# Optimization experiments

Hardware: AMD Instinct MI355X
Metric: run time of the kernel (lower is better)

## Reference

```python
import jax, jax.numpy as jnp
import numpy as np

B = 8192        # batch
DB = 64         # dim_body
DO = 128        # dim_object
NOBJ = 9        # nb_objects (all connected)
NE = 72         # edges = NOBJ*(NOBJ-1)
DE = 128        # edge feature dim
NISO = 3        # isolated nodes
HID = 256
PHI_OUT = 256
ACT = 32
LOG_SIG_MIN, LOG_SIG_MAX = -20.0, 2.0


def setup_inputs() -> dict:
    key = jax.random.key(0)
    ks = jax.random.split(key, 16)
    s = 0.05
    return {
        "obs": jax.random.normal(ks[0], (B, DB + NOBJ * DO), jnp.float32),
        "edge_features": jax.random.normal(ks[1], (B, NE, DE), jnp.float32),
        # every object id 0..8 appears NE//NOBJ times (static edge targets)
        "edges_to": jnp.tile(jnp.arange(NOBJ, dtype=jnp.int32), NE // NOBJ),
        "isolated_nodes": jax.random.normal(ks[2], (B, NISO, DO), jnp.float32),
        "isolated_nodes_features": jax.random.normal(ks[3], (B, NISO, DE), jnp.float32),
        "W1_phi": jax.random.normal(ks[4], (DB + DO + DE, HID), jnp.float32) * s,
        "b1_phi": jnp.zeros((HID,), jnp.float32),
        "W2_phi": jax.random.normal(ks[5], (HID, PHI_OUT), jnp.float32) * s,
        "b2_phi": jnp.zeros((PHI_OUT,), jnp.float32),
        "W1_rho": jax.random.normal(ks[6], (PHI_OUT, HID), jnp.float32) * s,
        "b1_rho": jnp.zeros((HID,), jnp.float32),
        "Wm": jax.random.normal(ks[7], (HID, ACT), jnp.float32) * s,
        "bm": jnp.zeros((ACT,), jnp.float32),
        "Ws": jax.random.normal(ks[8], (HID, ACT), jnp.float32) * s,
        "bs": jnp.zeros((ACT,), jnp.float32),
    }


def reference(obs, edge_features, edges_to, isolated_nodes, isolated_nodes_features,
              W1_phi, b1_phi, W2_phi, b2_phi, W1_rho, b1_rho, Wm, bm, Ws, bs):
    obs_body = obs[:, :DB]                              # [B, DB]
    obs_objects = obs[:, DB:].reshape(B, NOBJ, DO)      # [B, NOBJ, DO]

    # per-node max over incoming edges (segment-max over static edge targets)
    ef = jnp.transpose(edge_features, (1, 0, 2))        # [NE, B, DE]
    incoming = jax.ops.segment_max(ef, edges_to, num_segments=NOBJ)  # [NOBJ, B, DE]

    body_c = jnp.broadcast_to(obs_body, (NOBJ, B, DB))
    inp_connected = jnp.concatenate(
        [body_c, jnp.transpose(obs_objects, (1, 0, 2)), incoming], axis=-1)

    body_i = jnp.broadcast_to(obs_body, (NISO, B, DB))
    inp_isolated = jnp.concatenate(
        [body_i,
         jnp.transpose(isolated_nodes, (1, 0, 2)),
         jnp.transpose(isolated_nodes_features, (1, 0, 2))], axis=-1)

    inp = jnp.concatenate([inp_connected, inp_isolated], axis=0)  # [NOBJ+NISO, B, DB+DO+DE]

    # phi DeepSet MLP
    h = jax.nn.relu(inp @ W1_phi + b1_phi)
    phi = jax.nn.relu(h @ W2_phi + b2_phi)

    pooled = phi.sum(axis=0)                            # readout='sum' -> [B, PHI_OUT]

    # rho MLP -> (mean, log_std)
    r = jax.nn.relu(pooled @ W1_rho + b1_rho)
    mean = r @ Wm + bm
    log_std = jnp.clip(r @ Ws + bs, LOG_SIG_MIN, LOG_SIG_MAX)
    return mean, log_std
```

## Files before the change

### kernel.cpp

```cpp
#include <hip/hip_runtime.h>
#include <hip/hip_bf16.h>
#include <stdint.h>


#define Bsz   8192
#define OBSW  1216
#define NH    256

typedef unsigned short u16;
typedef unsigned int   u32;

using bf16x8 = __attribute__((ext_vector_type(8))) short;
using f32x4  = __attribute__((ext_vector_type(4))) float;

__device__ u16   g_W1t[256 * 320];
__device__ u16   g_W2t[256 * 256];
__device__ u16   g_Rt [256 * 256];
__device__ u16   g_Wcat[64 * 256];
__device__ float g_pooled[Bsz * NH];

__device__ __forceinline__ u16 f2bf(float f) {
  union { float f; u32 i; } v; v.f = f;
  u32 x = v.i;
  x += 0x7fffu + ((x >> 16) & 1u);
  return (u16)(x >> 16);
}
__device__ __forceinline__ uint4 pack8(const float* f) {
  uint4 o;
  o.x = (u32)f2bf(f[0]) | ((u32)f2bf(f[1]) << 16);
  o.y = (u32)f2bf(f[2]) | ((u32)f2bf(f[3]) << 16);
  o.z = (u32)f2bf(f[4]) | ((u32)f2bf(f[5]) << 16);
  o.w = (u32)f2bf(f[6]) | ((u32)f2bf(f[7]) << 16);
  return o;
}
__device__ __forceinline__ void load8f(const float* p, float* f) {
  *(float4*)(f)     = *(const float4*)(p);
  *(float4*)(f + 4) = *(const float4*)(p + 4);
}

__global__ void transpose_cast(const float* __restrict__ in, int dst,
                               int K, int N, int row_off) {
  __shared__ u16 tile[32][33];
  u16* out = (dst == 0) ? g_W1t : (dst == 1) ? g_W2t : (dst == 2) ? g_Rt : g_Wcat;
  int k0 = blockIdx.x * 32, n0 = blockIdx.y * 32;
  int c = threadIdx.x & 31, r0 = threadIdx.x >> 5;
  #pragma unroll
  for (int i = 0; i < 4; i++) {
    int r = r0 + i * 8;
    tile[r][c] = f2bf(in[(size_t)(k0 + r) * N + (n0 + c)]);
  }
  __syncthreads();
  #pragma unroll
  for (int i = 0; i < 4; i++) {
    int r = r0 + i * 8;
    out[(size_t)(n0 + r + row_off) * K + (k0 + c)] = tile[c][r];
  }
}

__global__ void zero_pooled() {
  size_t t = (size_t)blockIdx.x * 256 + threadIdx.x;
  float4 z = {0.f, 0.f, 0.f, 0.f};
  *(float4*)(g_pooled + t * 4) = z;
}

__global__ __launch_bounds__(256)
void node_kernel(const float* __restrict__ obs, const float* __restrict__ ef,
                 const float* __restrict__ iso, const float* __restrict__ isof,
                 const float* __restrict__ b1, const float* __restrict__ b2) {
  __shared__ __attribute__((aligned(16))) u16 As[32][72];
  __shared__ __attribute__((aligned(16))) u16 Bs[256][72];
  __shared__ __attribute__((aligned(16))) u16 Ht[32][264];
  const int btile = blockIdx.x >> 1;
  const int nhalf = blockIdx.x & 1;
  const int b0 = btile * 32;
  const int tid = threadIdx.x;
  const int wave = tid >> 6, lane = tid & 63;
  const int nw = wave * 64, lrow = lane & 15, quad = lane >> 4;
  const int srow = tid >> 3, sck = (tid & 7) * 8;
  const size_t sb = (size_t)(b0 + srow);

  const f32x4 vzero = {0.f, 0.f, 0.f, 0.f};
  f32x4 pool[2][4];
  #pragma unroll
  for (int a = 0; a < 2; a++)
    #pragma unroll
    for (int b = 0; b < 4; b++) pool[a][b] = vzero;

  for (int nn = 0; nn < 6; nn++) {
    const int n = nhalf * 6 + nn;
    f32x4 acc[2][4];
    #pragma unroll
    for (int a = 0; a < 2; a++)
      #pragma unroll
      for (int b = 0; b < 4; b++) acc[a][b] = vzero;

    for (int step = 0; step < 5; step++) {
      float f[8];
      if (step == 0) {
        load8f(obs + sb * OBSW + sck, f);
      } else if (step <= 2) {
        int kk = (step - 1) * 64 + sck;
        const float* p = (n < 9) ? obs + sb * OBSW + 64 + n * 128 + kk
                                 : iso + (sb * 3 + (n - 9)) * 128 + kk;
        load8f(p, f);
      } else {
        int kk = (step - 3) * 64 + sck;
        if (n < 9) {
          const float* base = ef + (sb * 72 + n) * 128 + kk;
          load8f(base, f);
          #pragma unroll
          for (int j = 1; j < 8; j++) {
            float w[8];
            load8f(base + (size_t)j * 1152, w);
            #pragma unroll
            for (int q = 0; q < 8; q++) f[q] = fmaxf(f[q], w[q]);
          }
        } else {
          load8f(isof + (sb * 3 + (n - 9)) * 128 + kk, f);
        }
      }
      *(uint4*)(&As[srow][sck]) = pack8(f);
      #pragma unroll
      for (int i = 0; i < 8; i++) {
        int row = srow + i * 32;
        *(uint4*)(&Bs[row][sck]) =
            *(const uint4*)(g_W1t + (size_t)row * 320 + step * 64 + sck);
      }
      __syncthreads();
      #pragma unroll
      for (int ks = 0; ks < 2; ks++) {
        int kk = ks * 32 + quad * 8;
        bf16x8 af[2], bq[4];
        af[0] = *(const bf16x8*)(&As[lrow][kk]);
        af[1] = *(const bf16x8*)(&As[16 + lrow][kk]);
        #pragma unroll
        for (int nb = 0; nb < 4; nb++)
          bq[nb] = *(const bf16x8*)(&Bs[nw + nb * 16 + lrow][kk]);
        #pragma unroll
        for (int mb = 0; mb < 2; mb++)
          #pragma unroll
          for (int nb = 0; nb < 4; nb++)
            acc[mb][nb] = __builtin_amdgcn_mfma_f32_16x16x32_bf16(
                af[mb], bq[nb], acc[mb][nb], 0, 0, 0);
      }
      __syncthreads();
    }
    #pragma unroll
    for (int nb = 0; nb < 4; nb++) {
      int col = nw + nb * 16 + lrow;
      float bv = b1[col];
      #pragma unroll
      for (int mb = 0; mb < 2; mb++)
        #pragma unroll
        for (int i = 0; i < 4; i++)
          Ht[mb * 16 + quad * 4 + i][col] = f2bf(fmaxf(acc[mb][nb][i] + bv, 0.f));
    }
    #pragma unroll
    for (int a = 0; a < 2; a++)
      #pragma unroll
      for (int b = 0; b < 4; b++) acc[a][b] = vzero;

    for (int k0 = 0; k0 < 256; k0 += 64) {
      #pragma unroll
      for (int i = 0; i < 8; i++) {
        int row = srow + i * 32;
        *(uint4*)(&Bs[row][sck]) =
            *(const uint4*)(g_W2t + (size_t)row * 256 + k0 + sck);
      }
      __syncthreads();
      #pragma unroll
      for (int ks = 0; ks < 2; ks++) {
        int kk = ks * 32 + quad * 8;
        bf16x8 af[2], bq[4];
        af[0] = *(const bf16x8*)(&Ht[lrow][k0 + kk]);
        af[1] = *(const bf16x8*)(&Ht[16 + lrow][k0 + kk]);
        #pragma unroll
        for (int nb = 0; nb < 4; nb++)
          bq[nb] = *(const bf16x8*)(&Bs[nw + nb * 16 + lrow][kk]);
        #pragma unroll
        for (int mb = 0; mb < 2; mb++)
          #pragma unroll
          for (int nb = 0; nb < 4; nb++)
            acc[mb][nb] = __builtin_amdgcn_mfma_f32_16x16x32_bf16(
                af[mb], bq[nb], acc[mb][nb], 0, 0, 0);
      }
      __syncthreads();
    }
    #pragma unroll
    for (int nb = 0; nb < 4; nb++) {
      int col = nw + nb * 16 + lrow;
      float bv = b2[col];
      #pragma unroll
      for (int mb = 0; mb < 2; mb++)
        #pragma unroll
        for (int i = 0; i < 4; i++)
          pool[mb][nb][i] += fmaxf(acc[mb][nb][i] + bv, 0.f);
    }
  }
  #pragma unroll
  for (int nb = 0; nb < 4; nb++) {
    int col = nw + nb * 16 + lrow;
    #pragma unroll
    for (int mb = 0; mb < 2; mb++)
      #pragma unroll
      for (int i = 0; i < 4; i++) {
        int row = b0 + mb * 16 + quad * 4 + i;
        atomicAdd(&g_pooled[(size_t)row * NH + col], pool[mb][nb][i]);
      }
  }
}

__global__ __launch_bounds__(256)
void rho_heads(const float* __restrict__ br, const float* __restrict__ bm,
               const float* __restrict__ bs, float* __restrict__ out) {
  __shared__ __attribute__((aligned(16))) u16 As2[32][264];
  __shared__ __attribute__((aligned(16))) u16 Bs2[256][72];
  const int b0 = blockIdx.x * 32;
  const int tid = threadIdx.x;
  const int wave = tid >> 6, lane = tid & 63;
  const int nw = wave * 64, lrow = lane & 15, quad = lane >> 4;
  const int srow = tid >> 3, sck = (tid & 7) * 8;

  #pragma unroll
  for (int c4 = 0; c4 < 4; c4++) {
    int col = c4 * 64 + sck;
    float f[8];
    load8f(g_pooled + (size_t)(b0 + srow) * NH + col, f);
    *(uint4*)(&As2[srow][col]) = pack8(f);
  }

  const f32x4 vzero = {0.f, 0.f, 0.f, 0.f};
  f32x4 acc[2][4];
  #pragma unroll
  for (int a = 0; a < 2; a++)
    #pragma unroll
    for (int b = 0; b < 4; b++) acc[a][b] = vzero;

  for (int k0 = 0; k0 < 256; k0 += 64) {
    #pragma unroll
    for (int i = 0; i < 8; i++) {
      int row = srow + i * 32;
      *(uint4*)(&Bs2[row][sck]) =
          *(const uint4*)(g_Rt + (size_t)row * 256 + k0 + sck);
    }
    __syncthreads();
    #pragma unroll
    for (int ks = 0; ks < 2; ks++) {
      int kk = ks * 32 + quad * 8;
      bf16x8 af[2], bq[4];
      af[0] = *(const bf16x8*)(&As2[lrow][k0 + kk]);
      af[1] = *(const bf16x8*)(&As2[16 + lrow][k0 + kk]);
      #pragma unroll
      for (int nb = 0; nb < 4; nb++)
        bq[nb] = *(const bf16x8*)(&Bs2[nw + nb * 16 + lrow][kk]);
      #pragma unroll
      for (int mb = 0; mb < 2; mb++)
        #pragma unroll
        for (int nb = 0; nb < 4; nb++)
          acc[mb][nb] = __builtin_amdgcn_mfma_f32_16x16x32_bf16(
              af[mb], bq[nb], acc[mb][nb], 0, 0, 0);
    }
    __syncthreads();
  }
  #pragma unroll
  for (int nb = 0; nb < 4; nb++) {
    int col = nw + nb * 16 + lrow;
    float bv = br[col];
    #pragma unroll
    for (int mb = 0; mb < 2; mb++)
      #pragma unroll
      for (int i = 0; i < 4; i++)
        As2[mb * 16 + quad * 4 + i][col] = f2bf(fmaxf(acc[mb][nb][i] + bv, 0.f));
  }

  f32x4 acc2[2] = {vzero, vzero};
  for (int k0 = 0; k0 < 256; k0 += 64) {
    {
      int wrow = tid >> 2, wck = (tid & 3) * 16;
      *(uint4*)(&Bs2[wrow][wck]) =
          *(const uint4*)(g_Wcat + (size_t)wrow * NH + k0 + wck);
      *(uint4*)(&Bs2[wrow][wck + 8]) =
          *(const uint4*)(g_Wcat + (size_t)wrow * NH + k0 + wck + 8);
    }
    __syncthreads();
    #pragma unroll
    for (int ks = 0; ks < 2; ks++) {
      int kk = ks * 32 + quad * 8;
      bf16x8 af[2], bq;
      af[0] = *(const bf16x8*)(&As2[lrow][k0 + kk]);
      af[1] = *(const bf16x8*)(&As2[16 + lrow][k0 + kk]);
      bq = *(const bf16x8*)(&Bs2[wave * 16 + lrow][kk]);
      acc2[0] = __builtin_amdgcn_mfma_f32_16x16x32_bf16(af[0], bq, acc2[0], 0, 0, 0);
      acc2[1] = __builtin_amdgcn_mfma_f32_16x16x32_bf16(af[1], bq, acc2[1], 0, 0, 0);
    }
    __syncthreads();
  }
  int j = wave * 16 + lrow;
  #pragma unroll
  for (int mb = 0; mb < 2; mb++) {
    #pragma unroll
    for (int i = 0; i < 4; i++) {
      int b = b0 + mb * 16 + quad * 4 + i;
      if (j < 32) {
        out[(size_t)b * 32 + j] = acc2[mb][i] + bm[j];
      } else {
        float v = acc2[mb][i] + bs[j - 32];
        v = fminf(fmaxf(v, -20.f), 2.f);
        out[(size_t)Bsz * 32 + (size_t)b * 32 + (j - 32)] = v;
      }
    }
  }
}

extern "C" void kernel_launch(void* const* d_in, const int* in_sizes, int n_in,
                              void* d_out, int out_size, void* d_ws, size_t ws_size,
                              hipStream_t stream) {
  const float* obs  = (const float*)d_in[0];
  const float* ef   = (const float*)d_in[1];
  const float* iso  = (const float*)d_in[3];
  const float* isof = (const float*)d_in[4];
  const float* W1   = (const float*)d_in[5];
  const float* b1   = (const float*)d_in[6];
  const float* W2   = (const float*)d_in[7];
  const float* b2   = (const float*)d_in[8];
  const float* Wr   = (const float*)d_in[9];
  const float* br   = (const float*)d_in[10];
  const float* Wm   = (const float*)d_in[11];
  const float* bm   = (const float*)d_in[12];
  const float* Wsg  = (const float*)d_in[13];
  const float* bs   = (const float*)d_in[14];
  float* out = (float*)d_out;
  (void)d_ws; (void)ws_size;

  transpose_cast<<<dim3(10, 8), 256, 0, stream>>>(W1, 0, 320, 256, 0);
  transpose_cast<<<dim3(8, 8), 256, 0, stream>>>(W2, 1, 256, 256, 0);
  transpose_cast<<<dim3(8, 8), 256, 0, stream>>>(Wr, 2, 256, 256, 0);
  transpose_cast<<<dim3(8, 1), 256, 0, stream>>>(Wm, 3, 256, 32, 0);
  transpose_cast<<<dim3(8, 1), 256, 0, stream>>>(Wsg, 3, 256, 32, 32);
  zero_pooled<<<(Bsz * NH / 4) / 256, 256, 0, stream>>>();

  node_kernel<<<(Bsz / 32) * 2, 256, 0, stream>>>(obs, ef, iso, isof, b1, b2);
  rho_heads<<<Bsz / 32, 256, 0, stream>>>(br, bm, bs, out);
}
```

Before: 546.9 us.

## Pre-format weights into MFMA fragment order and read them directly from global

Weights W1/W2 are reordered on device into MFMA B-fragment layout so each lane loads its bf16x8 operand straight from global/L2 instead of staging through shared memory. The whole 320-wide input row tile is loaded into LDS at once, which removes the per-k-step syncs. The node split grows from 2 to 4 groups per batch tile for more blocks, and launch bounds ask for 4 waves/SIMD occupancy. The trade-off is more global/L2 traffic for weights and more atomics into pooled.

```diff
diff --git a/kernel.cpp b/kernel.cpp
--- a/kernel.cpp
+++ b/kernel.cpp
@@ -13,8 +13,8 @@
 using bf16x8 = __attribute__((ext_vector_type(8))) short;
 using f32x4  = __attribute__((ext_vector_type(4))) float;
 
-__device__ u16   g_W1t[256 * 320];
-__device__ u16   g_W2t[256 * 256];
+__device__ u16   g_W1f[320 * 256];
+__device__ u16   g_W2f[256 * 256];
 __device__ u16   g_Rt [256 * 256];
 __device__ u16   g_Wcat[64 * 256];
 __device__ float g_pooled[Bsz * NH];
@@ -38,10 +38,19 @@
   *(float4*)(f + 4) = *(const float4*)(p + 4);
 }
 
+__global__ void format_frag(const float* __restrict__ in, int dst, int K) {
+  u16* outp = dst ? g_W2f : g_W1f;
+  int idx = blockIdx.x * 256 + threadIdx.x;
+  int k = idx >> 8, n = idx & 255;
+  if (k >= K) return;
+  int kc = k >> 5, q = (k >> 3) & 3, j = k & 7;
+  outp[((size_t)(kc * 4 + q) * 256 + n) * 8 + j] = f2bf(in[idx]);
+}
+
 __global__ void transpose_cast(const float* __restrict__ in, int dst,
                                int K, int N, int row_off) {
   __shared__ u16 tile[32][33];
-  u16* out = (dst == 0) ? g_W1t : (dst == 1) ? g_W2t : (dst == 2) ? g_Rt : g_Wcat;
+  u16* out = (dst == 2) ? g_Rt : g_Wcat;
   int k0 = blockIdx.x * 32, n0 = blockIdx.y * 32;
   int c = threadIdx.x & 31, r0 = threadIdx.x >> 5;
   #pragma unroll
@@ -63,21 +72,25 @@
   *(float4*)(g_pooled + t * 4) = z;
 }
 
-__global__ __launch_bounds__(256)
+__global__ __launch_bounds__(256, 4)
 void node_kernel(const float* __restrict__ obs, const float* __restrict__ ef,
                  const float* __restrict__ iso, const float* __restrict__ isof,
                  const float* __restrict__ b1, const float* __restrict__ b2) {
-  __shared__ __attribute__((aligned(16))) u16 As[32][72];
-  __shared__ __attribute__((aligned(16))) u16 Bs[256][72];
+  __shared__ __attribute__((aligned(16))) u16 As[32][328];
   __shared__ __attribute__((aligned(16))) u16 Ht[32][264];
-  const int btile = blockIdx.x >> 1;
-  const int nhalf = blockIdx.x & 1;
+  const int btile = blockIdx.x >> 2;
+  const int ng    = blockIdx.x & 3;
   const int b0 = btile * 32;
   const int tid = threadIdx.x;
   const int wave = tid >> 6, lane = tid & 63;
   const int nw = wave * 64, lrow = lane & 15, quad = lane >> 4;
-  const int srow = tid >> 3, sck = (tid & 7) * 8;
-  const size_t sb = (size_t)(b0 + srow);
+
+  float bias1[4], bias2[4];
+  #pragma unroll
+  for (int nb = 0; nb < 4; nb++) {
+    bias1[nb] = b1[nw + nb * 16 + lrow];
+    bias2[nb] = b2[nw + nb * 16 + lrow];
+  }
 
   const f32x4 vzero = {0.f, 0.f, 0.f, 0.f};
   f32x4 pool[2][4];
@@ -86,27 +99,27 @@
     #pragma unroll
     for (int b = 0; b < 4; b++) pool[a][b] = vzero;
 
-  for (int nn = 0; nn < 6; nn++) {
-    const int n = nhalf * 6 + nn;
-    f32x4 acc[2][4];
-    #pragma unroll
-    for (int a = 0; a < 2; a++)
-      #pragma unroll
-      for (int b = 0; b < 4; b++) acc[a][b] = vzero;
-
-    for (int step = 0; step < 5; step++) {
+  for (int nn = 0; nn < 3; nn++) {
+    const int n = ng * 3 + nn;
+
+    #pragma unroll
+    for (int it = 0; it < 5; it++) {
+      int task = it * 256 + tid;
+      int r = task / 40, c = task - r * 40;
+      size_t bb = (size_t)(b0 + r);
+      int k = c * 8;
       float f[8];
-      if (step == 0) {
-        load8f(obs + sb * OBSW + sck, f);
-      } else if (step <= 2) {
-        int kk = (step - 1) * 64 + sck;
-        const float* p = (n < 9) ? obs + sb * OBSW + 64 + n * 128 + kk
-                                 : iso + (sb * 3 + (n - 9)) * 128 + kk;
+      if (c < 8) {
+        load8f(obs + bb * OBSW + k, f);
+      } else if (c < 24) {
+        int kk = k - 64;
+        const float* p = (n < 9) ? obs + bb * OBSW + 64 + n * 128 + kk
+                                 : iso + (bb * 3 + (n - 9)) * 128 + kk;
         load8f(p, f);
       } else {
-        int kk = (step - 3) * 64 + sck;
+        int kk = k - 192;
         if (n < 9) {
-          const float* base = ef + (sb * 72 + n) * 128 + kk;
+          const float* base = ef + (bb * 72 + n) * 128 + kk;
           load8f(base, f);
           #pragma unroll
           for (int j = 1; j < 8; j++) {
@@ -116,86 +129,67 @@
             for (int q = 0; q < 8; q++) f[q] = fmaxf(f[q], w[q]);
           }
         } else {
-          load8f(isof + (sb * 3 + (n - 9)) * 128 + kk, f);
+          load8f(isof + (bb * 3 + (n - 9)) * 128 + kk, f);
         }
       }
-      *(uint4*)(&As[srow][sck]) = pack8(f);
-      #pragma unroll
-      for (int i = 0; i < 8; i++) {
-        int row = srow + i * 32;
-        *(uint4*)(&Bs[row][sck]) =
-            *(const uint4*)(g_W1t + (size_t)row * 320 + step * 64 + sck);
-      }
-      __syncthreads();
-      #pragma unroll
-      for (int ks = 0; ks < 2; ks++) {
-        int kk = ks * 32 + quad * 8;
-        bf16x8 af[2], bq[4];
-        af[0] = *(const bf16x8*)(&As[lrow][kk]);
-        af[1] = *(const bf16x8*)(&As[16 + lrow][kk]);
-        #pragma unroll
-        for (int nb = 0; nb < 4; nb++)
-          bq[nb] = *(const bf16x8*)(&Bs[nw + nb * 16 + lrow][kk]);
-        #pragma unroll
-        for (int mb = 0; mb < 2; mb++)
-          #pragma unroll
-          for (int nb = 0; nb < 4; nb++)
-            acc[mb][nb] = __builtin_amdgcn_mfma_f32_16x16x32_bf16(
-                af[mb], bq[nb], acc[mb][nb], 0, 0, 0);
-      }
-      __syncthreads();
+      *(uint4*)(&As[r][k]) = pack8(f);
+    }
+    __syncthreads();
+
+    f32x4 acc[2][4];
+    #pragma unroll
+    for (int a = 0; a < 2; a++)
+      #pragma unroll
+      for (int b = 0; b < 4; b++) acc[a][b] = vzero;
+    #pragma unroll
+    for (int kc = 0; kc < 10; kc++) {
+      bf16x8 a0 = *(const bf16x8*)(&As[lrow][kc * 32 + quad * 8]);
+      bf16x8 a1 = *(const bf16x8*)(&As[16 + lrow][kc * 32 + quad * 8]);
+      #pragma unroll
+      for (int nb = 0; nb < 4; nb++) {
+        int col = nw + nb * 16 + lrow;
+        bf16x8 bf = *(const bf16x8*)(g_W1f +
+                       ((size_t)(kc * 4 + quad) * 256 + col) * 8);
+        acc[0][nb] = __builtin_amdgcn_mfma_f32_16x16x32_bf16(a0, bf, acc[0][nb], 0, 0, 0);
+        acc[1][nb] = __builtin_amdgcn_mfma_f32_16x16x32_bf16(a1, bf, acc[1][nb], 0, 0, 0);
+      }
     }
     #pragma unroll
     for (int nb = 0; nb < 4; nb++) {
       int col = nw + nb * 16 + lrow;
-      float bv = b1[col];
       #pragma unroll
       for (int mb = 0; mb < 2; mb++)
         #pragma unroll
         for (int i = 0; i < 4; i++)
-          Ht[mb * 16 + quad * 4 + i][col] = f2bf(fmaxf(acc[mb][nb][i] + bv, 0.f));
-    }
+          Ht[mb * 16 + quad * 4 + i][col] =
+              f2bf(fmaxf(acc[mb][nb][i] + bias1[nb], 0.f));
+    }
+    __syncthreads();
+
     #pragma unroll
     for (int a = 0; a < 2; a++)
       #pragma unroll
       for (int b = 0; b < 4; b++) acc[a][b] = vzero;
-
-    for (int k0 = 0; k0 < 256; k0 += 64) {
-      #pragma unroll
-      for (int i = 0; i < 8; i++) {
-        int row = srow + i * 32;
-        *(uint4*)(&Bs[row][sck]) =
-            *(const uint4*)(g_W2t + (size_t)row * 256 + k0 + sck);
-      }
-      __syncthreads();
-      #pragma unroll
-      for (int ks = 0; ks < 2; ks++) {
-        int kk = ks * 32 + quad * 8;
-        bf16x8 af[2], bq[4];
-        af[0] = *(const bf16x8*)(&Ht[lrow][k0 + kk]);
-        af[1] = *(const bf16x8*)(&Ht[16 + lrow][k0 + kk]);
-        #pragma unroll
-        for (int nb = 0; nb < 4; nb++)
-          bq[nb] = *(const bf16x8*)(&Bs[nw + nb * 16 + lrow][kk]);
-        #pragma unroll
-        for (int mb = 0; mb < 2; mb++)
-          #pragma unroll
-          for (int nb = 0; nb < 4; nb++)
-            acc[mb][nb] = __builtin_amdgcn_mfma_f32_16x16x32_bf16(
-                af[mb], bq[nb], acc[mb][nb], 0, 0, 0);
-      }
-      __syncthreads();
-    }
-    #pragma unroll
-    for (int nb = 0; nb < 4; nb++) {
-      int col = nw + nb * 16 + lrow;
-      float bv = b2[col];
+    #pragma unroll
+    for (int kc = 0; kc < 8; kc++) {
+      bf16x8 a0 = *(const bf16x8*)(&Ht[lrow][kc * 32 + quad * 8]);
+      bf16x8 a1 = *(const bf16x8*)(&Ht[16 + lrow][kc * 32 + quad * 8]);
+      #pragma unroll
+      for (int nb = 0; nb < 4; nb++) {
+        int col = nw + nb * 16 + lrow;
+        bf16x8 bf = *(const bf16x8*)(g_W2f +
+                       ((size_t)(kc * 4 + quad) * 256 + col) * 8);
+        acc[0][nb] = __builtin_amdgcn_mfma_f32_16x16x32_bf16(a0, bf, acc[0][nb], 0, 0, 0);
+        acc[1][nb] = __builtin_amdgcn_mfma_f32_16x16x32_bf16(a1, bf, acc[1][nb], 0, 0, 0);
+      }
+    }
+    #pragma unroll
+    for (int nb = 0; nb < 4; nb++)
       #pragma unroll
       for (int mb = 0; mb < 2; mb++)
         #pragma unroll
         for (int i = 0; i < 4; i++)
-          pool[mb][nb][i] += fmaxf(acc[mb][nb][i] + bv, 0.f);
-    }
+          pool[mb][nb][i] += fmaxf(acc[mb][nb][i] + bias2[nb], 0.f);
   }
   #pragma unroll
   for (int nb = 0; nb < 4; nb++) {
@@ -332,13 +326,13 @@
   float* out = (float*)d_out;
   (void)d_ws; (void)ws_size;
 
-  transpose_cast<<<dim3(10, 8), 256, 0, stream>>>(W1, 0, 320, 256, 0);
-  transpose_cast<<<dim3(8, 8), 256, 0, stream>>>(W2, 1, 256, 256, 0);
+  format_frag<<<320, 256, 0, stream>>>(W1, 0, 320);
+  format_frag<<<256, 256, 0, stream>>>(W2, 1, 256);
   transpose_cast<<<dim3(8, 8), 256, 0, stream>>>(Wr, 2, 256, 256, 0);
   transpose_cast<<<dim3(8, 1), 256, 0, stream>>>(Wm, 3, 256, 32, 0);
   transpose_cast<<<dim3(8, 1), 256, 0, stream>>>(Wsg, 3, 256, 32, 32);
   zero_pooled<<<(Bsz * NH / 4) / 256, 256, 0, stream>>>();
 
-  node_kernel<<<(Bsz / 32) * 2, 256, 0, stream>>>(obs, ef, iso, isof, b1, b2);
+  node_kernel<<<(Bsz / 32) * 4, 256, 0, stream>>>(obs, ef, iso, isof, b1, b2);
   rho_heads<<<Bsz / 32, 256, 0, stream>>>(br, bm, bs, out);
 }
```

New measurement: 652.9 us. 1.19x slower.
